# Performance work log

Hardware: AMD Instinct MI355X
Metric: run time of the kernel (lower is better)

Reference implementation:

```python
import jax, jax.numpy as jnp
import numpy as np

EMBED_DIM = 768
NUM_HEADS = 12
SEGMENT_LENGTHS = (2048, 4096, 8192)
DILATION_RATES = (1, 2, 4)
LN_EPS = 1e-5


def setup_inputs() -> dict:
    rng = jax.random.key(0)
    ks = jax.random.split(rng, 6)
    B, S, E = 2, 8192, EMBED_DIM
    xavier = (2.0 / (E + E)) ** 0.5  # xavier_normal std for square fan-in/out
    return {
        "query": jax.random.normal(ks[0], (B, S, E), jnp.float32),
        "key": jax.random.normal(ks[1], (B, S, E), jnp.float32),
        "value": jax.random.normal(ks[2], (B, S, E), jnp.float32),
        "qkv_w": jax.random.normal(ks[3], (3 * E, E), jnp.float32) * xavier,
        "qkv_b": jnp.zeros((3 * E,), jnp.float32),
        "ln_w": jnp.ones((E,), jnp.float32),
        "ln_b": jnp.zeros((E,), jnp.float32),
        "out_w": jax.random.normal(ks[4], (E, E), jnp.float32) * xavier,
        "out_b": jnp.zeros((E,), jnp.float32),
    }


def _dilated_attention(q, k, v):
    # q,k,v: [b, n, h, d].  Heads are partitioned across the
    # (segment_length, dilation_rate) groups; within each group the sequence
    # is split into segments of length s and subsampled with stride r at
    # offset (i % r); plain softmax attention runs inside each dilated segment.
    b, n, h, d = q.shape
    G = len(SEGMENT_LENGTHS)
    g = h // G
    scale = 1.0 / np.sqrt(d)
    out = jnp.zeros_like(q)
    for i, (s, r) in enumerate(zip(SEGMENT_LENGTHS, DILATION_RATES)):
        off = i % r
        h0, h1 = i * g, (i + 1) * g
        m = n // s
        def seg(x):
            # [b, n, g, d] -> [b, m, s/r, g, d]
            return x[:, :, h0:h1].reshape(b, m, s, g, d)[:, :, off::r]
        qi, ki, vi = seg(q), seg(k), seg(v)
        scores = jnp.einsum("bmqgd,bmkgd->bmgqk", qi, ki) * scale
        p = jax.nn.softmax(scores, axis=-1)
        xi = jnp.einsum("bmgqk,bmkgd->bmqgd", p, vi)
        seg_out = jnp.zeros((b, m, s, g, d), q.dtype).at[:, :, off::r].set(xi)
        out = out.at[:, :, h0:h1].set(seg_out.reshape(b, n, g, d))
    return out / G


def reference(query, key, value, qkv_w, qkv_b, ln_w, ln_b, out_w, out_b):
    B, S, E = query.shape
    H = NUM_HEADS
    d = E // H
    # fused QKV projection (cross-attention path of the fused projection)
    q = (query @ qkv_w[:E].T + qkv_b[:E]).reshape(B, S, H, d)
    k = (key @ qkv_w[E:2 * E].T + qkv_b[E:2 * E]).reshape(B, S, H, d)
    v = (value @ qkv_w[2 * E:].T + qkv_b[2 * E:]).reshape(B, S, H, d)
    x = _dilated_attention(q, k, v).reshape(B, S, E)
    # MAGNETO layer norm before output projection
    mu = jnp.mean(x, axis=-1, keepdims=True)
    var = jnp.mean(jnp.square(x - mu), axis=-1, keepdims=True)
    x = (x - mu) * jax.lax.rsqrt(var + LN_EPS) * ln_w + ln_b
    return x @ out_w.T + out_b
```

## Files before the change

### kernel.cpp

```cpp
#include <hip/hip_runtime.h>
#include <hip/hip_bf16.h>
#include <math.h>

typedef __bf16 bf16_t;
typedef __bf16 bf16x8 __attribute__((ext_vector_type(8)));
typedef __bf16 bf16x4 __attribute__((ext_vector_type(4)));
typedef float f32x4 __attribute__((ext_vector_type(4)));

__device__ __forceinline__ void async_ld16(const void* g, void* l) {
  __builtin_amdgcn_global_load_lds(
      (const __attribute__((address_space(1))) unsigned int*)g,
      (__attribute__((address_space(3))) unsigned int*)l, 16, 0, 0);
}

#define BATCH 2
#define SEQ   8192
#define EMB   768
#define NHEAD 12
#define HD    64
#define TOK   (BATCH*SEQ)
#define GATH_PER_B 57344

__device__ __forceinline__ int headoff(int h) {
  int g = h >> 2;
  int base = (g == 0) ? 0 : ((g == 1) ? 32768 : 49152);
  return base + (h & 3) * (8192 >> g);
}

__device__ __forceinline__ float fast_exp2(float x) {
#if __has_builtin(__builtin_amdgcn_exp2f)
  return __builtin_amdgcn_exp2f(x);
#else
  return exp2f(x);
#endif
}

__global__ void k_cast(const float* __restrict__ in, bf16_t* __restrict__ out, int n) {
  int i = (blockIdx.x * blockDim.x + threadIdx.x) * 8;
  if (i < n) {
    float4 a = *(const float4*)(in + i);
    float4 b = *(const float4*)(in + i + 4);
    __attribute__((aligned(16))) bf16_t o[8] = {
        (bf16_t)a.x, (bf16_t)a.y, (bf16_t)a.z, (bf16_t)a.w,
        (bf16_t)b.x, (bf16_t)b.y, (bf16_t)b.z, (bf16_t)b.w};
    *(uint4*)(out + i) = *(uint4*)o;
  }
}

__global__ __launch_bounds__(256, 3)
void k_gemm_qkv(const float* __restrict__ qf, const float* __restrict__ kf,
                const float* __restrict__ vf, const bf16_t* __restrict__ wqkv,
                const float* __restrict__ qkv_bias,
                bf16_t* __restrict__ Qg, bf16_t* __restrict__ Kg, bf16_t* __restrict__ Vb) {
  const int N = 768, K = 768;
  int id = blockIdx.x;
  int wid = (id & 7) * 288 + (id >> 3);
  int z = wid / 768;
  int rem = wid - z * 768;
  int ytile = rem / 6;
  int xtile = rem - ytile * 6;
  int m0 = ytile * 128, n0 = xtile * 128;

  const float* A = (z == 0) ? qf : (z == 1) ? kf : vf;
  const bf16_t* W = wqkv + (size_t)z * N * K;
  const float* bias = qkv_bias + z * N;

  __shared__ float  As[2][128][32];
  __shared__ bf16_t Bs[2][128][32];

  int tid = threadIdx.x;
  int wave = tid >> 6, lane = tid & 63;
  int q = lane >> 4, c = lane & 15;
  int cx = c & 7;
  int wm = (wave & 1) * 64, wn = (wave >> 1) * 64;

  auto stage = [&](int k0, int bsel) {
#pragma unroll
    for (int it = 0; it < 4; ++it) {
      int ch = tid + it * 256;
      int row = ch >> 3, pc = ch & 7, lc = pc ^ (row & 7);
      async_ld16(A + (size_t)(m0 + row) * K + k0 + lc * 4,
                 (float*)&As[bsel][0][0] + ch * 4);
    }
#pragma unroll
    for (int it = 0; it < 2; ++it) {
      int ch = tid + it * 256;
      int row = ch >> 2, kb8 = (ch & 3) << 3;
      async_ld16(W + (size_t)(n0 + row) * K + k0 + kb8, &Bs[bsel][row][kb8]);
    }
  };

  f32x4 acc[4][4];
#pragma unroll
  for (int i = 0; i < 4; i++)
#pragma unroll
    for (int j = 0; j < 4; j++) acc[i][j] = (f32x4){0.f, 0.f, 0.f, 0.f};

  int s0 = (q * 2) ^ cx, s1 = (q * 2 + 1) ^ cx;

  stage(0, 0);
#pragma unroll 2
  for (int kt = 0; kt < 24; ++kt) {
    int cur = kt & 1;
    __syncthreads();
    if (kt + 1 < 24) stage((kt + 1) * 32, cur ^ 1);
    bf16x8 af[4], bfr[4];
#pragma unroll
    for (int mi = 0; mi < 4; mi++) {
      const float* ar = &As[cur][wm + mi * 16 + c][0];
      f32x4 a0 = *(const f32x4*)(ar + s0 * 4);
      f32x4 a1 = *(const f32x4*)(ar + s1 * 4);
      bf16x8 t;
#pragma unroll
      for (int j = 0; j < 4; j++) { t[j] = (bf16_t)a0[j]; t[4 + j] = (bf16_t)a1[j]; }
      af[mi] = t;
    }
#pragma unroll
    for (int nj = 0; nj < 4; nj++) bfr[nj] = *(const bf16x8*)&Bs[cur][wn + nj * 16 + c][q * 8];
#pragma unroll
    for (int mi = 0; mi < 4; mi++)
#pragma unroll
      for (int nj = 0; nj < 4; nj++)
        acc[mi][nj] = __builtin_amdgcn_mfma_f32_16x16x32_bf16(af[mi], bfr[nj], acc[mi][nj], 0, 0, 0);
  }

  if (z == 2) {
#pragma unroll
    for (int mi = 0; mi < 4; mi++)
#pragma unroll
      for (int nj = 0; nj < 4; nj++)
#pragma unroll
        for (int rg = 0; rg < 4; rg++) {
          int row = m0 + wm + mi * 16 + q * 4 + rg;
          int col = n0 + wn + nj * 16 + c;
          Vb[(size_t)row * N + col] = (bf16_t)(acc[mi][nj][rg] + bias[col]);
        }
  } else {
    bf16_t* dst = (z == 0) ? Qg : Kg;
    float qscale = (z == 0) ? 0.125f * 1.44269504088896f : 1.0f;
#pragma unroll
    for (int mi = 0; mi < 4; mi++)
#pragma unroll
      for (int nj = 0; nj < 4; nj++) {
        int e = n0 + wn + nj * 16 + c;
        int h = e >> 6, dim = e & 63, g2 = h >> 2;
        int rm1 = (1 << g2) - 1, sh = 11 + g2;
        int smask = (2048 << g2) - 1;
        int ho = headoff(h);
#pragma unroll
        for (int rg = 0; rg < 4; rg++) {
          int row = m0 + wm + mi * 16 + q * 4 + rg;
          float v = (acc[mi][nj][rg] + bias[e]) * qscale;
          int bb = row >> 13, p = row & 8191;
          int t = (p & smask) - g2;
          if (t >= 0 && (t & rm1) == 0) {
            int jj = (p >> sh) * 2048 + (t >> g2);
            dst[(size_t)(bb * GATH_PER_B + ho + jj) * HD + dim] = (bf16_t)v;
          }
        }
      }
  }
}

__global__ __launch_bounds__(256, 4)
void k_gemm_out(const bf16_t* __restrict__ A, const bf16_t* __restrict__ W,
                const float* __restrict__ bias, float* __restrict__ C) {
  const int N = 768, K = 768;
  int id = blockIdx.x;
  int wid = (id & 7) * 96 + (id >> 3);
  int ytile = wid / 6;
  int xtile = wid - ytile * 6;
  int m0 = ytile * 128, n0 = xtile * 128;

  __shared__ bf16_t As[2][128][32];
  __shared__ bf16_t Bs[2][128][32];

  int tid = threadIdx.x;
  int wave = tid >> 6, lane = tid & 63;
  int q = lane >> 4, c = lane & 15;
  int wm = (wave & 1) * 64, wn = (wave >> 1) * 64;

  auto stage = [&](int k0, int bsel) {
#pragma unroll
    for (int it = 0; it < 2; ++it) {
      int ch = tid + it * 256;
      int row = ch >> 2, kb8 = (ch & 3) << 3;
      async_ld16(A + (size_t)(m0 + row) * K + k0 + kb8, &As[bsel][row][kb8]);
      async_ld16(W + (size_t)(n0 + row) * K + k0 + kb8, &Bs[bsel][row][kb8]);
    }
  };

  f32x4 acc[4][4];
#pragma unroll
  for (int i = 0; i < 4; i++)
#pragma unroll
    for (int j = 0; j < 4; j++) acc[i][j] = (f32x4){0.f, 0.f, 0.f, 0.f};

  stage(0, 0);
#pragma unroll 2
  for (int kt = 0; kt < 24; ++kt) {
    int cur = kt & 1;
    __syncthreads();
    if (kt + 1 < 24) stage((kt + 1) * 32, cur ^ 1);
    bf16x8 af[4], bfr[4];
#pragma unroll
    for (int mi = 0; mi < 4; mi++) af[mi] = *(const bf16x8*)&As[cur][wm + mi * 16 + c][q * 8];
#pragma unroll
    for (int nj = 0; nj < 4; nj++) bfr[nj] = *(const bf16x8*)&Bs[cur][wn + nj * 16 + c][q * 8];
#pragma unroll
    for (int mi = 0; mi < 4; mi++)
#pragma unroll
      for (int nj = 0; nj < 4; nj++)
        acc[mi][nj] = __builtin_amdgcn_mfma_f32_16x16x32_bf16(af[mi], bfr[nj], acc[mi][nj], 0, 0, 0);
  }
#pragma unroll
  for (int mi = 0; mi < 4; mi++)
#pragma unroll
    for (int nj = 0; nj < 4; nj++)
#pragma unroll
      for (int rg = 0; rg < 4; rg++) {
        int row = m0 + wm + mi * 16 + q * 4 + rg;
        int col = n0 + wn + nj * 16 + c;
        C[(size_t)row * N + col] = acc[mi][nj][rg] + bias[col];
      }
}

__global__ __launch_bounds__(256)
void k_gather_v(const bf16_t* __restrict__ Vb, bf16_t* __restrict__ Vt) {
  int h = blockIdx.y, b = blockIdx.z;
  int g = h >> 2;
  int L = 8192 >> g;
  int jj0 = blockIdx.x * 64;
  if (jj0 >= L) return;
  int s = 2048 << g;
  int hb = b * GATH_PER_B + headoff(h);
  int tid = threadIdx.x;

  __shared__ bf16_t tile[64][72];

#pragma unroll
  for (int it = 0; it < 2; ++it) {
    int ch = tid + it * 256;
    int rowl = ch >> 3, db = (ch & 7) << 3;
    int jj = jj0 + rowl;
    int p = (jj >> 11) * s + g + ((jj & 2047) << g);
    *(uint4*)&tile[rowl][db] = *(const uint4*)(Vb + ((size_t)(b * SEQ + p)) * EMB + h * HD + db);
  }
  __syncthreads();
  int dim = tid >> 2, sub = tid & 3;
  __attribute__((aligned(16))) bf16_t tmp[16];
#pragma unroll
  for (int sl = 0; sl < 16; sl++) {
    int t = sub * 16 + sl;
    int pos = (t & 3) * 16 + (t >> 2);
    tmp[sl] = tile[pos][dim];
  }
  size_t vdst = ((size_t)hb) * HD + (size_t)dim * L + jj0 + sub * 16;
  *(uint4*)(Vt + vdst) = *(uint4*)&tmp[0];
  *(uint4*)(Vt + vdst + 8) = *(uint4*)&tmp[8];
}

__global__ __launch_bounds__(256, 2)
void k_attn(const bf16_t* __restrict__ Qg, const bf16_t* __restrict__ Kg,
            const bf16_t* __restrict__ Vt, bf16_t* __restrict__ xattn) {
  int u = blockIdx.x;
  int seg = u % 56, qt = u / 56;
  int b = seg / 28, t = seg % 28;
  int g, h, si;
  if (t < 16)      { g = 0; h = t >> 2;              si = t & 3; }
  else if (t < 24) { g = 1; h = 4 + ((t - 16) >> 1); si = (t - 16) & 1; }
  else             { g = 2; h = 8 + (t - 24);        si = 0; }
  int L = 8192 >> g, s = 2048 << g;
  int hb = b * GATH_PER_B + headoff(h);
  int jj0 = si * 2048 + qt * 128;
  int kvbase = si * 2048;

  __shared__ bf16_t Ps[128][64];
  __shared__ bf16_t Ks[2][128][64];
  __shared__ bf16_t Vs[2][64][128];

  int tid = threadIdx.x, wave = tid >> 6, lane = tid & 63;
  int q = lane >> 4, c = lane & 15;
  int cx = c & 7;
  int wm = wave * 32;

  auto stageK = [&](int kt, int bsel) {
#pragma unroll
    for (int it = 0; it < 4; ++it) {
      int ch = tid + it * 256;
      int row = ch >> 3, pc = ch & 7, lc = pc ^ (row & 7);
      async_ld16(Kg + ((size_t)(hb + kvbase + kt * 128 + row)) * HD + lc * 8,
                 &Ks[bsel][0][0] + ch * 8);
    }
  };
  auto stageV = [&](int kt, int bsel) {
#pragma unroll
    for (int it = 0; it < 4; ++it) {
      int ch = tid + it * 256;
      int dim = ch >> 4, pc = ch & 15, lc = pc ^ (dim & 7);
      async_ld16(Vt + ((size_t)hb) * HD + (size_t)dim * L + kvbase + kt * 128 + lc * 8,
                 &Vs[bsel][0][0] + ch * 8);
    }
  };

  bf16_t* Qs = &Ps[0][0];
#pragma unroll
  for (int it = 0; it < 4; ++it) {
    int ch = tid + it * 256;
    int row = ch >> 3, pc = ch & 7, lc = pc ^ (row & 7);
    async_ld16(Qg + ((size_t)(hb + jj0 + row)) * HD + lc * 8, Qs + ch * 8);
  }
  stageK(0, 0);
  stageV(0, 0);
  __syncthreads();

  bf16x8 aq[2][2];
#pragma unroll
  for (int mi = 0; mi < 2; mi++)
#pragma unroll
    for (int kq = 0; kq < 2; kq++) {
      int pch = (kq * 4 + q) ^ cx;
      aq[mi][kq] = *(const bf16x8*)(Qs + (size_t)(wm + mi * 16 + c) * HD + pch * 8);
    }

  float lrow[2][4];
  f32x4 O[2][4];
#pragma unroll
  for (int mi = 0; mi < 2; mi++)
#pragma unroll
    for (int rg = 0; rg < 4; rg++) lrow[mi][rg] = 0.f;
#pragma unroll
  for (int mi = 0; mi < 2; mi++)
#pragma unroll
    for (int vd = 0; vd < 4; vd++) O[mi][vd] = (f32x4){0.f, 0.f, 0.f, 0.f};

#pragma unroll 2
  for (int kt = 0; kt < 16; ++kt) {
    int cur = kt & 1;
    if (kt < 15) {
      stageK(kt + 1, cur ^ 1);
      stageV(kt + 1, cur ^ 1);
    }

    f32x4 Sv[2][8];
#pragma unroll
    for (int mi = 0; mi < 2; mi++)
#pragma unroll
      for (int nj = 0; nj < 8; nj++) Sv[mi][nj] = (f32x4){0.f, 0.f, 0.f, 0.f};
#pragma unroll
    for (int kq = 0; kq < 2; kq++) {
      int pch = (kq * 4 + q) ^ cx;
      bf16x8 bk[8];
#pragma unroll
      for (int nj = 0; nj < 8; nj++) bk[nj] = *(const bf16x8*)&Ks[cur][nj * 16 + c][pch * 8];
#pragma unroll
      for (int mi = 0; mi < 2; mi++)
#pragma unroll
        for (int nj = 0; nj < 8; nj++)
          Sv[mi][nj] = __builtin_amdgcn_mfma_f32_16x16x32_bf16(aq[mi][kq], bk[nj], Sv[mi][nj], 0, 0, 0);
    }

#pragma unroll
    for (int half = 0; half < 2; ++half) {
#pragma unroll
      for (int mi = 0; mi < 2; mi++)
#pragma unroll
        for (int rg = 0; rg < 4; rg++) {
          bf16x4 p4;
          float rs = 0.f;
#pragma unroll
          for (int j = 0; j < 4; j++) {
            float p = fast_exp2(Sv[mi][half * 4 + j][rg]);
            rs += p;
            p4[j] = (bf16_t)p;
          }
          lrow[mi][rg] += rs;
          int row = wm + mi * 16 + q * 4 + rg;
          int u8 = c ^ ((row & 7) << 1);
          *(bf16x4*)((char*)&Ps[row][0] + u8 * 8) = p4;
        }
#pragma unroll
      for (int kk2 = 0; kk2 < 2; ++kk2) {
        bf16x8 ap[2], bv[4];
#pragma unroll
        for (int mi = 0; mi < 2; mi++) {
          int u8 = (kk2 * 8 + q * 2) ^ (cx << 1);
          ap[mi] = *(const bf16x8*)((char*)&Ps[wm + mi * 16 + c][0] + u8 * 8);
        }
#pragma unroll
        for (int vd = 0; vd < 4; vd++) {
          int pch = (half * 8 + kk2 * 4 + q) ^ cx;
          bv[vd] = *(const bf16x8*)&Vs[cur][vd * 16 + c][pch * 8];
        }
#pragma unroll
        for (int mi = 0; mi < 2; mi++)
#pragma unroll
          for (int vd = 0; vd < 4; vd++)
            O[mi][vd] = __builtin_amdgcn_mfma_f32_16x16x32_bf16(ap[mi], bv[vd], O[mi][vd], 0, 0, 0);
      }
    }
    __syncthreads();
  }

  const float inv3 = 1.0f / 3.0f;
#pragma unroll
  for (int mi = 0; mi < 2; mi++)
#pragma unroll
    for (int rg = 0; rg < 4; rg++) {
      float l = lrow[mi][rg];
#pragma unroll
      for (int d = 1; d < 16; d <<= 1) l += __shfl_xor(l, d, 64);
      float invl = inv3 / l;
      int jj = jj0 + wm + mi * 16 + q * 4 + rg;
      int p = si * s + g + ((jj & 2047) << g);
      size_t base = ((size_t)(b * SEQ + p)) * EMB + h * HD;
#pragma unroll
      for (int vd = 0; vd < 4; vd++)
        xattn[base + vd * 16 + c] = (bf16_t)(O[mi][vd][rg] * invl);
    }
}

__global__ __launch_bounds__(256)
void k_ln(const bf16_t* __restrict__ x, const float* __restrict__ lnw,
          const float* __restrict__ lnb, bf16_t* __restrict__ y) {
  int wave = threadIdx.x >> 6, lane = threadIdx.x & 63;
  int row = blockIdx.x * 4 + wave;
  const bf16_t* xr = x + (size_t)row * EMB + lane * 12;
  bf16x4 v4[3];
#pragma unroll
  for (int j = 0; j < 3; j++) v4[j] = *(const bf16x4*)(xr + j * 4);
  float v[12], s = 0.f, s2 = 0.f;
#pragma unroll
  for (int j = 0; j < 12; j++) {
    v[j] = (float)v4[j >> 2][j & 3];
    s += v[j];
    s2 += v[j] * v[j];
  }
#pragma unroll
  for (int d = 1; d < 64; d <<= 1) { s += __shfl_xor(s, d, 64); s2 += __shfl_xor(s2, d, 64); }
  float mu = s * (1.f / 768.f);
  float var = s2 * (1.f / 768.f) - mu * mu;
  float rstd = rsqrtf(var + 1e-5f);
  const float4* wr = (const float4*)(lnw + lane * 12);
  const float4* br = (const float4*)(lnb + lane * 12);
  bf16_t* yr = y + (size_t)row * EMB + lane * 12;
#pragma unroll
  for (int j = 0; j < 3; j++) {
    float4 w = wr[j], bb = br[j];
    bf16x4 o;
    o[0] = (bf16_t)((v[j * 4 + 0] - mu) * rstd * w.x + bb.x);
    o[1] = (bf16_t)((v[j * 4 + 1] - mu) * rstd * w.y + bb.y);
    o[2] = (bf16_t)((v[j * 4 + 2] - mu) * rstd * w.z + bb.z);
    o[3] = (bf16_t)((v[j * 4 + 3] - mu) * rstd * w.w + bb.w);
    *(bf16x4*)(yr + j * 4) = o;
  }
}

extern "C" void kernel_launch(void* const* d_in, const int* in_sizes, int n_in,
                              void* d_out, int out_size, void* d_ws, size_t ws_size,
                              hipStream_t stream) {
  const float* query = (const float*)d_in[0];
  const float* key   = (const float*)d_in[1];
  const float* value = (const float*)d_in[2];
  const float* qkv_w = (const float*)d_in[3];
  const float* qkv_b = (const float*)d_in[4];
  const float* ln_w  = (const float*)d_in[5];
  const float* ln_b  = (const float*)d_in[6];
  const float* out_w = (const float*)d_in[7];
  const float* out_b = (const float*)d_in[8];
  float* out = (float*)d_out;

  char* ws = (char*)d_ws;
  const size_t A = (size_t)TOK * EMB * 2;
  bf16_t* xattn = (bf16_t*)(ws + 0 * A);
  bf16_t* xnorm = (bf16_t*)(ws + 1 * A);
  bf16_t* Vt    = (bf16_t*)(ws + 2 * A);
  bf16_t* Vb    = (bf16_t*)(ws + 3 * A);
  bf16_t* Qg    = (bf16_t*)(ws + 4 * A);
  bf16_t* Kg    = (bf16_t*)(ws + 5 * A);
  bf16_t* wqkv  = (bf16_t*)(ws + 6 * A);
  bf16_t* wout  = (bf16_t*)(ws + 6 * A + (size_t)2304 * 768 * 2);

  k_cast<<<864, 256, 0, stream>>>(qkv_w, wqkv, 2304 * 768);
  k_cast<<<288, 256, 0, stream>>>(out_w, wout, 768 * 768);

  k_gemm_qkv<<<2304, 256, 0, stream>>>(query, key, value, wqkv, qkv_b, Qg, Kg, Vb);

  dim3 gg(128, 12, 2);
  k_gather_v<<<gg, 256, 0, stream>>>(Vb, Vt);

  hipMemsetAsync(xattn, 0, A, stream);
  k_attn<<<896, 256, 0, stream>>>(Qg, Kg, Vt, xattn);

  k_ln<<<4096, 256, 0, stream>>>(xattn, ln_w, ln_b, xnorm);

  k_gemm_out<<<768, 256, 0, stream>>>(xnorm, wout, out_b, out);
}
```

Measured before the change: 433.8 us.

## Stage QKV GEMM A tile through registers as bf16 instead of fp32 LDS

```diff
diff --git a/kernel.cpp b/kernel.cpp
--- a/kernel.cpp
+++ b/kernel.cpp
@@ -47,7 +47,7 @@
   }
 }
 
-__global__ __launch_bounds__(256, 3)
+__global__ __launch_bounds__(256, 4)
 void k_gemm_qkv(const float* __restrict__ qf, const float* __restrict__ kf,
                 const float* __restrict__ vf, const bf16_t* __restrict__ wqkv,
                 const float* __restrict__ qkv_bias,
@@ -65,23 +65,35 @@
   const bf16_t* W = wqkv + (size_t)z * N * K;
   const float* bias = qkv_bias + z * N;
 
-  __shared__ float  As[2][128][32];
+  __shared__ bf16_t As[2][128][32];
   __shared__ bf16_t Bs[2][128][32];
 
   int tid = threadIdx.x;
   int wave = tid >> 6, lane = tid & 63;
   int q = lane >> 4, c = lane & 15;
-  int cx = c & 7;
   int wm = (wave & 1) * 64, wn = (wave >> 1) * 64;
 
-  auto stage = [&](int k0, int bsel) {
-#pragma unroll
-    for (int it = 0; it < 4; ++it) {
-      int ch = tid + it * 256;
-      int row = ch >> 3, pc = ch & 7, lc = pc ^ (row & 7);
-      async_ld16(A + (size_t)(m0 + row) * K + k0 + lc * 4,
-                 (float*)&As[bsel][0][0] + ch * 4);
-    }
+  int chA = tid * 2;
+  int rowA = chA >> 2, c8A = (chA & 3) << 3;
+
+  f32x4 rA[2][2];
+  auto loadA = [&](int k0) {
+    const float* src = A + (size_t)(m0 + rowA) * K + k0 + c8A;
+    rA[0][0] = *(const f32x4*)src;
+    rA[0][1] = *(const f32x4*)(src + 4);
+    rA[1][0] = *(const f32x4*)(src + 8);
+    rA[1][1] = *(const f32x4*)(src + 12);
+  };
+  auto writeA = [&](int bsel) {
+#pragma unroll
+    for (int u = 0; u < 2; ++u) {
+      bf16x8 t;
+#pragma unroll
+      for (int j = 0; j < 4; j++) { t[j] = (bf16_t)rA[u][0][j]; t[4 + j] = (bf16_t)rA[u][1][j]; }
+      *(bf16x8*)&As[bsel][rowA][c8A + u * 8] = t;
+    }
+  };
+  auto stageW = [&](int k0, int bsel) {
 #pragma unroll
     for (int it = 0; it < 2; ++it) {
       int ch = tid + it * 256;
@@ -96,25 +108,21 @@
 #pragma unroll
     for (int j = 0; j < 4; j++) acc[i][j] = (f32x4){0.f, 0.f, 0.f, 0.f};
 
-  int s0 = (q * 2) ^ cx, s1 = (q * 2 + 1) ^ cx;
-
-  stage(0, 0);
+  loadA(0);
+  stageW(0, 0);
+  writeA(0);
+  __syncthreads();
+
 #pragma unroll 2
   for (int kt = 0; kt < 24; ++kt) {
-    int cur = kt & 1;
-    __syncthreads();
-    if (kt + 1 < 24) stage((kt + 1) * 32, cur ^ 1);
+    int cur = kt & 1, nxt = cur ^ 1;
+    if (kt + 1 < 24) {
+      stageW((kt + 1) * 32, nxt);
+      loadA((kt + 1) * 32);
+    }
     bf16x8 af[4], bfr[4];
 #pragma unroll
-    for (int mi = 0; mi < 4; mi++) {
-      const float* ar = &As[cur][wm + mi * 16 + c][0];
-      f32x4 a0 = *(const f32x4*)(ar + s0 * 4);
-      f32x4 a1 = *(const f32x4*)(ar + s1 * 4);
-      bf16x8 t;
-#pragma unroll
-      for (int j = 0; j < 4; j++) { t[j] = (bf16_t)a0[j]; t[4 + j] = (bf16_t)a1[j]; }
-      af[mi] = t;
-    }
+    for (int mi = 0; mi < 4; mi++) af[mi] = *(const bf16x8*)&As[cur][wm + mi * 16 + c][q * 8];
 #pragma unroll
     for (int nj = 0; nj < 4; nj++) bfr[nj] = *(const bf16x8*)&Bs[cur][wn + nj * 16 + c][q * 8];
 #pragma unroll
@@ -122,6 +130,8 @@
 #pragma unroll
       for (int nj = 0; nj < 4; nj++)
         acc[mi][nj] = __builtin_amdgcn_mfma_f32_16x16x32_bf16(af[mi], bfr[nj], acc[mi][nj], 0, 0, 0);
+    if (kt + 1 < 24) writeA(nxt);
+    __syncthreads();
   }
 
   if (z == 2) {
```

Result: no change. 429.1 us (-1.1%).
